# Performance work log

Measured on AMD Instinct MI355X. Metric: run time of the kernel, lower is better.

The kernel has to match this reference:

```python
import jax, jax.numpy as jnp
import numpy as np

B = 2048          # batch
F = 32            # input feature size
H = 512           # lstm hidden size
BN = 64           # autoencoder bottleneck
OUT = 8           # final dense output size
SEQ_LEN = 128
LOOK_AHEAD = 32
RS, RE = 0, 8     # replace_start, replace_end (RE-RS == OUT)


def setup_inputs() -> dict:
    key = jax.random.key(0)
    ks = jax.random.split(key, 16)
    s = lambda k, shape: (jax.random.normal(k, shape, jnp.float32) * 0.05)
    return {
        'x': jax.random.normal(ks[0], (B, SEQ_LEN + LOOK_AHEAD, F), jnp.float32),
        # layer-0 LSTMCell (input F)
        'Wih0': s(ks[1], (F, 4 * H)), 'Whh0': s(ks[2], (H, 4 * H)),
        'bih0': s(ks[3], (4 * H,)),   'bhh0': s(ks[4], (4 * H,)),
        # layer-1 LSTMCell (input H)
        'Wih1': s(ks[5], (H, 4 * H)), 'Whh1': s(ks[6], (H, 4 * H)),
        'bih1': s(ks[7], (4 * H,)),   'bhh1': s(ks[8], (4 * H,)),
        # discretizing autoencoder: 2H -> BN -> 2H (shared across layers)
        'We': s(ks[9], (2 * H, BN)),  'be': s(ks[10], (BN,)),
        'Wd': s(ks[11], (BN, 2 * H)), 'bd': s(ks[12], (2 * H,)),
        # final dense H -> OUT
        'Wf': s(ks[13], (H, OUT)),    'bf': s(ks[14], (OUT,)),
    }


def _lstm_cell(x, h, c, Wih, Whh, bih, bhh):
    # torch.nn.LSTMCell gate order: i, f, g, o
    g = x @ Wih + bih + h @ Whh + bhh          # [B, 4H]
    i, f, gg, o = jnp.split(g, 4, axis=1)
    i, f, o = jax.nn.sigmoid(i), jax.nn.sigmoid(f), jax.nn.sigmoid(o)
    c2 = f * c + i * jnp.tanh(gg)
    return o * jnp.tanh(c2), c2


def _ae(z, We, be, Wd, bd):
    # bottleneck with straight-through rounding (discretization)
    b = jnp.tanh(z @ We + be)
    q = b + jax.lax.stop_gradient(jnp.round(b) - b)
    return q @ Wd + bd


def _layers_fwd(x_t, st, p):
    h0, c0, h1, c1 = st
    hc = _ae(jnp.concatenate([h0, c0], axis=1), p['We'], p['be'], p['Wd'], p['bd'])
    h0, c0 = jnp.split(hc, 2, axis=1)
    h0, c0 = _lstm_cell(x_t, h0, c0, p['Wih0'], p['Whh0'], p['bih0'], p['bhh0'])
    # dropout layer between stacked layers is identity in eval mode
    hc = _ae(jnp.concatenate([h1, c1], axis=1), p['We'], p['be'], p['Wd'], p['bd'])
    h1, c1 = jnp.split(hc, 2, axis=1)
    h1, c1 = _lstm_cell(h0, h1, c1, p['Wih1'], p['Whh1'], p['bih1'], p['bhh1'])
    return (h0, c0, h1, c1)


def reference(x, Wih0, Whh0, bih0, bhh0, Wih1, Whh1, bih1, bhh1,
              We, be, Wd, bd, Wf, bf):
    p = dict(Wih0=Wih0, Whh0=Whh0, bih0=bih0, bhh0=bhh0,
             Wih1=Wih1, Whh1=Whh1, bih1=bih1, bhh1=bhh1,
             We=We, be=be, Wd=Wd, bd=bd)
    bsz = x.shape[0]
    z = jnp.zeros((bsz, H), x.dtype)
    st = (z, z, z, z)

    # warm-up phase over seq_len observed steps
    def step1(st, x_t):
        return _layers_fwd(x_t, st, p), None
    st, _ = jax.lax.scan(step1, st, jnp.swapaxes(x[:, :SEQ_LEN], 0, 1))
    out0 = st[2] @ Wf + bf  # final dense on top-layer h

    def step2(carry, x_t):
        st, out = carry
        x_t = x_t.at[:, RS:RE].set(out)
        st = _layers_fwd(x_t, st, p)
        out = st[2] @ Wf + bf
        return (st, out), out
    (_, _), outs = jax.lax.scan(step2, (st, out0),
                                jnp.swapaxes(x[:, SEQ_LEN:SEQ_LEN + LOOK_AHEAD], 0, 1))

    # [B, 1 + look_ahead, OUT]
    return jnp.concatenate([out0[:, None, :], jnp.swapaxes(outs, 0, 1)], axis=1)
```

## Files before the change

kernel.cpp:

```cpp
#include <hip/hip_runtime.h>
#include <math.h>

#define NB    2048
#define FIN   32
#define HH    512
#define G4    2048
#define BNE   64
#define OUTD  8
#define SEQL  128
#define LOOK  32
#define TOT   (SEQL + LOOK)
#define TB    8
#define NTHR  512

__device__ __forceinline__ float sigf(float v) { return 1.0f / (1.0f + expf(-v)); }

#define GMAC4(A, W)                                                     \
  { A[0].x = fmaf((W).x, hv.x, A[0].x); A[0].y = fmaf((W).y, hv.x, A[0].y); \
    A[1].x = fmaf((W).x, hv.y, A[1].x); A[1].y = fmaf((W).y, hv.y, A[1].y); \
    A[2].x = fmaf((W).x, hv.z, A[2].x); A[2].y = fmaf((W).y, hv.z, A[2].y); \
    A[3].x = fmaf((W).x, hv.w, A[3].x); A[3].y = fmaf((W).y, hv.w, A[3].y); }

__global__ __launch_bounds__(NTHR)
void fused_rnn(const float* __restrict__ x,
               const float* __restrict__ Wih0, const float* __restrict__ Whh0,
               const float* __restrict__ bih0, const float* __restrict__ bhh0,
               const float* __restrict__ Wih1, const float* __restrict__ Whh1,
               const float* __restrict__ bih1, const float* __restrict__ bhh1,
               const float* __restrict__ We,   const float* __restrict__ be,
               const float* __restrict__ Wd,   const float* __restrict__ bd,
               const float* __restrict__ Wf,   const float* __restrict__ bf,
               float* __restrict__ out)
{
  __shared__ float sh0[HH][TB], sc0[HH][TB], sh1[HH][TB], sc1[HH][TB];
  __shared__ float tq[2][BNE][TB];
  __shared__ float sx[FIN][TB];
  __shared__ float sout[TB][OUTD];

  const int t  = threadIdx.x;
  const int b0 = blockIdx.x * TB;

  for (int i = t; i < HH * TB; i += NTHR) {
    (&sh0[0][0])[i] = 0.f; (&sc0[0][0])[i] = 0.f;
    (&sh1[0][0])[i] = 0.f; (&sc1[0][0])[i] = 0.f;
  }

  const int q  = t & 255;
  const int sh = t >> 8;
  const int s4 = 4 * sh;
  const int u0 = 2 * q;
  float2 bg0[4], bg1[4];
#pragma unroll
  for (int m = 0; m < 4; m++) {
    const int c = m * HH + u0;
    bg0[m] = make_float2(bih0[c] + bhh0[c], bih0[c + 1] + bhh0[c + 1]);
    bg1[m] = make_float2(bih1[c] + bhh1[c], bih1[c + 1] + bhh1[c + 1]);
  }

  const int ae = t >> 8, n = t & 63, sp = (t >> 6) & 3;

  const float bdx = bd[2 * t], bdy = bd[2 * t + 1];

  const double Athr = 0.5493061443340549;

  for (int step = 0; step < TOT; ++step) {
    __syncthreads();

    {
      const float* Sh = ae ? &sh1[0][0] : &sh0[0][0];
      const float* Sc = ae ? &sc1[0][0] : &sc0[0][0];
      double a0 = (double)be[n], a1 = a0;
      const float* weh = We + n;
#pragma unroll 4
      for (int k = 0; k < HH; k++) {
        const float2 zz = *(const float2*)&Sh[k * TB + 2 * sp];
        const double wv = (double)weh[(size_t)k * BNE];
        a0 = fma((double)zz.x, wv, a0);
        a1 = fma((double)zz.y, wv, a1);
      }
      const float* wec = We + (size_t)HH * BNE + n;
#pragma unroll 4
      for (int k = 0; k < HH; k++) {
        const float2 zz = *(const float2*)&Sc[k * TB + 2 * sp];
        const double wv = (double)wec[(size_t)k * BNE];
        a0 = fma((double)zz.x, wv, a0);
        a1 = fma((double)zz.y, wv, a1);
      }
      tq[ae][n][2 * sp]     = (a0 > Athr) ? 1.f : ((a0 < -Athr) ? -1.f : 0.f);
      tq[ae][n][2 * sp + 1] = (a1 > Athr) ? 1.f : ((a1 < -Athr) ? -1.f : 0.f);
    }
    __syncthreads();

    {
      float2 d0[TB], d1[TB];
#pragma unroll
      for (int s = 0; s < TB; s++) { d0[s] = make_float2(bdx, bdy); d1[s] = d0[s]; }
      const float* wd = Wd + 2 * t;
#pragma unroll 2
      for (int j = 0; j < BNE; j++) {
        const float2 w = *(const float2*)&wd[(size_t)j * (2 * HH)];
        const float4 qA0 = *(const float4*)&tq[0][j][0];
        const float4 qB0 = *(const float4*)&tq[0][j][4];
        const float4 qA1 = *(const float4*)&tq[1][j][0];
        const float4 qB1 = *(const float4*)&tq[1][j][4];
        d0[0].x = fmaf(qA0.x, w.x, d0[0].x); d0[0].y = fmaf(qA0.x, w.y, d0[0].y);
        d0[1].x = fmaf(qA0.y, w.x, d0[1].x); d0[1].y = fmaf(qA0.y, w.y, d0[1].y);
        d0[2].x = fmaf(qA0.z, w.x, d0[2].x); d0[2].y = fmaf(qA0.z, w.y, d0[2].y);
        d0[3].x = fmaf(qA0.w, w.x, d0[3].x); d0[3].y = fmaf(qA0.w, w.y, d0[3].y);
        d0[4].x = fmaf(qB0.x, w.x, d0[4].x); d0[4].y = fmaf(qB0.x, w.y, d0[4].y);
        d0[5].x = fmaf(qB0.y, w.x, d0[5].x); d0[5].y = fmaf(qB0.y, w.y, d0[5].y);
        d0[6].x = fmaf(qB0.z, w.x, d0[6].x); d0[6].y = fmaf(qB0.z, w.y, d0[6].y);
        d0[7].x = fmaf(qB0.w, w.x, d0[7].x); d0[7].y = fmaf(qB0.w, w.y, d0[7].y);
        d1[0].x = fmaf(qA1.x, w.x, d1[0].x); d1[0].y = fmaf(qA1.x, w.y, d1[0].y);
        d1[1].x = fmaf(qA1.y, w.x, d1[1].x); d1[1].y = fmaf(qA1.y, w.y, d1[1].y);
        d1[2].x = fmaf(qA1.z, w.x, d1[2].x); d1[2].y = fmaf(qA1.z, w.y, d1[2].y);
        d1[3].x = fmaf(qA1.w, w.x, d1[3].x); d1[3].y = fmaf(qA1.w, w.y, d1[3].y);
        d1[4].x = fmaf(qB1.x, w.x, d1[4].x); d1[4].y = fmaf(qB1.x, w.y, d1[4].y);
        d1[5].x = fmaf(qB1.y, w.x, d1[5].x); d1[5].y = fmaf(qB1.y, w.y, d1[5].y);
        d1[6].x = fmaf(qB1.z, w.x, d1[6].x); d1[6].y = fmaf(qB1.z, w.y, d1[6].y);
        d1[7].x = fmaf(qB1.w, w.x, d1[7].x); d1[7].y = fmaf(qB1.w, w.y, d1[7].y);
      }
      if (t < 256) {
        const int u = 2 * t;
        *(float4*)&sh0[u][0]     = make_float4(d0[0].x, d0[1].x, d0[2].x, d0[3].x);
        *(float4*)&sh0[u][4]     = make_float4(d0[4].x, d0[5].x, d0[6].x, d0[7].x);
        *(float4*)&sh0[u + 1][0] = make_float4(d0[0].y, d0[1].y, d0[2].y, d0[3].y);
        *(float4*)&sh0[u + 1][4] = make_float4(d0[4].y, d0[5].y, d0[6].y, d0[7].y);
        *(float4*)&sh1[u][0]     = make_float4(d1[0].x, d1[1].x, d1[2].x, d1[3].x);
        *(float4*)&sh1[u][4]     = make_float4(d1[4].x, d1[5].x, d1[6].x, d1[7].x);
        *(float4*)&sh1[u + 1][0] = make_float4(d1[0].y, d1[1].y, d1[2].y, d1[3].y);
        *(float4*)&sh1[u + 1][4] = make_float4(d1[4].y, d1[5].y, d1[6].y, d1[7].y);
      } else {
        const int u = 2 * t - HH;
        *(float4*)&sc0[u][0]     = make_float4(d0[0].x, d0[1].x, d0[2].x, d0[3].x);
        *(float4*)&sc0[u][4]     = make_float4(d0[4].x, d0[5].x, d0[6].x, d0[7].x);
        *(float4*)&sc0[u + 1][0] = make_float4(d0[0].y, d0[1].y, d0[2].y, d0[3].y);
        *(float4*)&sc0[u + 1][4] = make_float4(d0[4].y, d0[5].y, d0[6].y, d0[7].y);
        *(float4*)&sc1[u][0]     = make_float4(d1[0].x, d1[1].x, d1[2].x, d1[3].x);
        *(float4*)&sc1[u][4]     = make_float4(d1[4].x, d1[5].x, d1[6].x, d1[7].x);
        *(float4*)&sc1[u + 1][0] = make_float4(d1[0].y, d1[1].y, d1[2].y, d1[3].y);
        *(float4*)&sc1[u + 1][4] = make_float4(d1[4].y, d1[5].y, d1[6].y, d1[7].y);
      }
      if (t < FIN * TB) {
        int s = t >> 5, f = t & 31;
        float xv;
        if (step >= SEQL && f < OUTD) xv = sout[s][f];
        else xv = x[((size_t)(b0 + s) * TOT + step) * FIN + f];
        sx[f][s] = xv;
      }
    }
    __syncthreads();

    {
      float2 gI[4], gF[4], gG[4], gO[4];
#pragma unroll
      for (int i = 0; i < 4; i++) { gI[i] = bg0[0]; gF[i] = bg0[1]; gG[i] = bg0[2]; gO[i] = bg0[3]; }
      {
        const float* row = Wih0 + u0;
#pragma unroll 4
        for (int k = 0; k < FIN; k++, row += G4) {
          const float2 wI = *(const float2*)(row);
          const float2 wF = *(const float2*)(row + HH);
          const float2 wG = *(const float2*)(row + 2 * HH);
          const float2 wO = *(const float2*)(row + 3 * HH);
          const float4 hv = *(const float4*)&sx[k][s4];
          GMAC4(gI, wI); GMAC4(gF, wF); GMAC4(gG, wG); GMAC4(gO, wO);
        }
      }
      {
        const float* row = Whh0 + u0;
#pragma unroll 8
        for (int k = 0; k < HH; k++, row += G4) {
          const float2 wI = *(const float2*)(row);
          const float2 wF = *(const float2*)(row + HH);
          const float2 wG = *(const float2*)(row + 2 * HH);
          const float2 wO = *(const float2*)(row + 3 * HH);
          const float4 hv = *(const float4*)&sh0[k][s4];
          GMAC4(gI, wI); GMAC4(gF, wF); GMAC4(gG, wG); GMAC4(gO, wO);
        }
      }
      const float4 cA = *(const float4*)&sc0[u0][s4];
      const float4 cB = *(const float4*)&sc0[u0 + 1][s4];
      const float coldA[4] = { cA.x, cA.y, cA.z, cA.w };
      const float coldB[4] = { cB.x, cB.y, cB.z, cB.w };
      float4 hnA, hnB, cnA, cnB;
      float* hA = (float*)&hnA; float* hB = (float*)&hnB;
      float* cnAp = (float*)&cnA; float* cnBp = (float*)&cnB;
#pragma unroll
      for (int i = 0; i < 4; i++) {
        float ig = sigf(gI[i].x), fg = sigf(gF[i].x);
        float gt = tanhf(gG[i].x), og = sigf(gO[i].x);
        float c2 = fmaf(fg, coldA[i], ig * gt);
        cnAp[i] = c2; hA[i] = og * tanhf(c2);
        ig = sigf(gI[i].y); fg = sigf(gF[i].y);
        gt = tanhf(gG[i].y); og = sigf(gO[i].y);
        c2 = fmaf(fg, coldB[i], ig * gt);
        cnBp[i] = c2; hB[i] = og * tanhf(c2);
      }
      __syncthreads();
      *(float4*)&sh0[u0][s4]     = hnA;
      *(float4*)&sh0[u0 + 1][s4] = hnB;
      *(float4*)&sc0[u0][s4]     = cnA;
      *(float4*)&sc0[u0 + 1][s4] = cnB;
    }
    __syncthreads();

    {
      float2 gI[4], gF[4], gG[4], gO[4];
#pragma unroll
      for (int i = 0; i < 4; i++) { gI[i] = bg1[0]; gF[i] = bg1[1]; gG[i] = bg1[2]; gO[i] = bg1[3]; }
      {
        const float* row = Wih1 + u0;
#pragma unroll 8
        for (int k = 0; k < HH; k++, row += G4) {
          const float2 wI = *(const float2*)(row);
          const float2 wF = *(const float2*)(row + HH);
          const float2 wG = *(const float2*)(row + 2 * HH);
          const float2 wO = *(const float2*)(row + 3 * HH);
          const float4 hv = *(const float4*)&sh0[k][s4];
          GMAC4(gI, wI); GMAC4(gF, wF); GMAC4(gG, wG); GMAC4(gO, wO);
        }
      }
      {
        const float* row = Whh1 + u0;
#pragma unroll 8
        for (int k = 0; k < HH; k++, row += G4) {
          const float2 wI = *(const float2*)(row);
          const float2 wF = *(const float2*)(row + HH);
          const float2 wG = *(const float2*)(row + 2 * HH);
          const float2 wO = *(const float2*)(row + 3 * HH);
          const float4 hv = *(const float4*)&sh1[k][s4];
          GMAC4(gI, wI); GMAC4(gF, wF); GMAC4(gG, wG); GMAC4(gO, wO);
        }
      }
      const float4 cA = *(const float4*)&sc1[u0][s4];
      const float4 cB = *(const float4*)&sc1[u0 + 1][s4];
      const float coldA[4] = { cA.x, cA.y, cA.z, cA.w };
      const float coldB[4] = { cB.x, cB.y, cB.z, cB.w };
      float4 hnA, hnB, cnA, cnB;
      float* hA = (float*)&hnA; float* hB = (float*)&hnB;
      float* cnAp = (float*)&cnA; float* cnBp = (float*)&cnB;
#pragma unroll
      for (int i = 0; i < 4; i++) {
        float ig = sigf(gI[i].x), fg = sigf(gF[i].x);
        float gt = tanhf(gG[i].x), og = sigf(gO[i].x);
        float c2 = fmaf(fg, coldA[i], ig * gt);
        cnAp[i] = c2; hA[i] = og * tanhf(c2);
        ig = sigf(gI[i].y); fg = sigf(gF[i].y);
        gt = tanhf(gG[i].y); og = sigf(gO[i].y);
        c2 = fmaf(fg, coldB[i], ig * gt);
        cnBp[i] = c2; hB[i] = og * tanhf(c2);
      }
      __syncthreads();
      *(float4*)&sh1[u0][s4]     = hnA;
      *(float4*)&sh1[u0 + 1][s4] = hnB;
      *(float4*)&sc1[u0][s4]     = cnA;
      *(float4*)&sc1[u0 + 1][s4] = cnB;
    }

    if (step >= SEQL - 1) {
      __syncthreads();
      if (t < TB * OUTD) {
        int s = t >> 3, o = t & 7;
        float a = bf[o];
#pragma unroll 4
        for (int k = 0; k < HH; k++) a = fmaf(sh1[k][s], Wf[k * OUTD + o], a);
        sout[s][o] = a;
        int slot = step - (SEQL - 1);
        out[((size_t)(b0 + s) * (1 + LOOK) + slot) * OUTD + o] = a;
      }
    }
  }
}

extern "C" void kernel_launch(void* const* d_in, const int* in_sizes, int n_in,
                              void* d_out, int out_size, void* d_ws, size_t ws_size,
                              hipStream_t stream) {
  const float* x    = (const float*)d_in[0];
  const float* Wih0 = (const float*)d_in[1];
  const float* Whh0 = (const float*)d_in[2];
  const float* bih0 = (const float*)d_in[3];
  const float* bhh0 = (const float*)d_in[4];
  const float* Wih1 = (const float*)d_in[5];
  const float* Whh1 = (const float*)d_in[6];
  const float* bih1 = (const float*)d_in[7];
  const float* bhh1 = (const float*)d_in[8];
  const float* We   = (const float*)d_in[9];
  const float* be   = (const float*)d_in[10];
  const float* Wd   = (const float*)d_in[11];
  const float* bd   = (const float*)d_in[12];
  const float* Wf   = (const float*)d_in[13];
  const float* bf   = (const float*)d_in[14];

  fused_rnn<<<NB / TB, NTHR, 0, stream>>>(x, Wih0, Whh0, bih0, bhh0,
                                          Wih1, Whh1, bih1, bhh1,
                                          We, be, Wd, bd, Wf, bf,
                                          (float*)d_out);
}
```

Baseline: 92.00 ms.

## Double batch tile per block to 16 rows with 1024 threads and remap AE work

Raises the per-block batch tile from 8 to 16 samples and the block size from 512 to 1024 threads. The encoder and decoder thread mappings are reworked: each encoder thread now handles one sample for both layers, and each decoder thread produces one output column for all 16 samples, one layer after the other. The aim is to reuse every weight load from global memory across more batch rows, halving total weight traffic, at the cost of fewer blocks (128), doubled shared memory per block, and possible register pressure. The unseen LSTM gate section must also be consistent with the new TB and NTHR.

```diff
diff --git a/kernel.cpp b/kernel.cpp
--- a/kernel.cpp
+++ b/kernel.cpp
@@ -10,8 +10,8 @@
 #define SEQL  128
 #define LOOK  32
 #define TOT   (SEQL + LOOK)
-#define TB    8
-#define NTHR  512
+#define TB    16
+#define NTHR  1024
 
 __device__ __forceinline__ float sigf(float v) { return 1.0f / (1.0f + expf(-v)); }
 
@@ -33,7 +33,7 @@
                float* __restrict__ out)
 {
   __shared__ float sh0[HH][TB], sc0[HH][TB], sh1[HH][TB], sc1[HH][TB];
-  __shared__ float tq[2][BNE][TB];
+  __shared__ float sq[2][BNE][TB];
   __shared__ float sx[FIN][TB];
   __shared__ float sout[TB][OUTD];
 
@@ -46,8 +46,8 @@
   }
 
   const int q  = t & 255;
-  const int sh = t >> 8;
-  const int s4 = 4 * sh;
+  const int v  = t >> 8;
+  const int s4 = 4 * v;
   const int u0 = 2 * q;
   float2 bg0[4], bg1[4];
 #pragma unroll
@@ -57,9 +57,9 @@
     bg1[m] = make_float2(bih1[c] + bhh1[c], bih1[c + 1] + bhh1[c + 1]);
   }
 
-  const int ae = t >> 8, n = t & 63, sp = (t >> 6) & 3;
-
-  const float bdx = bd[2 * t], bdy = bd[2 * t + 1];
+  const int n = t & 63, sE = t >> 6;
+
+  const float bdv = bd[t];
 
   const double Athr = 0.5493061443340549;
 
@@ -67,79 +67,76 @@
     __syncthreads();
 
     {
-      const float* Sh = ae ? &sh1[0][0] : &sh0[0][0];
-      const float* Sc = ae ? &sc1[0][0] : &sc0[0][0];
       double a0 = (double)be[n], a1 = a0;
       const float* weh = We + n;
 #pragma unroll 4
       for (int k = 0; k < HH; k++) {
-        const float2 zz = *(const float2*)&Sh[k * TB + 2 * sp];
         const double wv = (double)weh[(size_t)k * BNE];
-        a0 = fma((double)zz.x, wv, a0);
-        a1 = fma((double)zz.y, wv, a1);
+        a0 = fma((double)sh0[k][sE], wv, a0);
+        a1 = fma((double)sh1[k][sE], wv, a1);
       }
       const float* wec = We + (size_t)HH * BNE + n;
 #pragma unroll 4
       for (int k = 0; k < HH; k++) {
-        const float2 zz = *(const float2*)&Sc[k * TB + 2 * sp];
         const double wv = (double)wec[(size_t)k * BNE];
-        a0 = fma((double)zz.x, wv, a0);
-        a1 = fma((double)zz.y, wv, a1);
-      }
-      tq[ae][n][2 * sp]     = (a0 > Athr) ? 1.f : ((a0 < -Athr) ? -1.f : 0.f);
-      tq[ae][n][2 * sp + 1] = (a1 > Athr) ? 1.f : ((a1 < -Athr) ? -1.f : 0.f);
-    }
-    __syncthreads();
-
-    {
-      float2 d0[TB], d1[TB];
-#pragma unroll
-      for (int s = 0; s < TB; s++) { d0[s] = make_float2(bdx, bdy); d1[s] = d0[s]; }
-      const float* wd = Wd + 2 * t;
+        a0 = fma((double)sc0[k][sE], wv, a0);
+        a1 = fma((double)sc1[k][sE], wv, a1);
+      }
+      sq[0][n][sE] = (a0 > Athr) ? 1.f : ((a0 < -Athr) ? -1.f : 0.f);
+      sq[1][n][sE] = (a1 > Athr) ? 1.f : ((a1 < -Athr) ? -1.f : 0.f);
+    }
+    __syncthreads();
+
+    {
+      const float* wd = Wd + t;
+      float d[TB];
+#pragma unroll
+      for (int s = 0; s < TB; s++) d[s] = bdv;
 #pragma unroll 2
       for (int j = 0; j < BNE; j++) {
-        const float2 w = *(const float2*)&wd[(size_t)j * (2 * HH)];
-        const float4 qA0 = *(const float4*)&tq[0][j][0];
-        const float4 qB0 = *(const float4*)&tq[0][j][4];
-        const float4 qA1 = *(const float4*)&tq[1][j][0];
-        const float4 qB1 = *(const float4*)&tq[1][j][4];
-        d0[0].x = fmaf(qA0.x, w.x, d0[0].x); d0[0].y = fmaf(qA0.x, w.y, d0[0].y);
-        d0[1].x = fmaf(qA0.y, w.x, d0[1].x); d0[1].y = fmaf(qA0.y, w.y, d0[1].y);
-        d0[2].x = fmaf(qA0.z, w.x, d0[2].x); d0[2].y = fmaf(qA0.z, w.y, d0[2].y);
-        d0[3].x = fmaf(qA0.w, w.x, d0[3].x); d0[3].y = fmaf(qA0.w, w.y, d0[3].y);
-        d0[4].x = fmaf(qB0.x, w.x, d0[4].x); d0[4].y = fmaf(qB0.x, w.y, d0[4].y);
-        d0[5].x = fmaf(qB0.y, w.x, d0[5].x); d0[5].y = fmaf(qB0.y, w.y, d0[5].y);
-        d0[6].x = fmaf(qB0.z, w.x, d0[6].x); d0[6].y = fmaf(qB0.z, w.y, d0[6].y);
-        d0[7].x = fmaf(qB0.w, w.x, d0[7].x); d0[7].y = fmaf(qB0.w, w.y, d0[7].y);
-        d1[0].x = fmaf(qA1.x, w.x, d1[0].x); d1[0].y = fmaf(qA1.x, w.y, d1[0].y);
-        d1[1].x = fmaf(qA1.y, w.x, d1[1].x); d1[1].y = fmaf(qA1.y, w.y, d1[1].y);
-        d1[2].x = fmaf(qA1.z, w.x, d1[2].x); d1[2].y = fmaf(qA1.z, w.y, d1[2].y);
-        d1[3].x = fmaf(qA1.w, w.x, d1[3].x); d1[3].y = fmaf(qA1.w, w.y, d1[3].y);
-        d1[4].x = fmaf(qB1.x, w.x, d1[4].x); d1[4].y = fmaf(qB1.x, w.y, d1[4].y);
-        d1[5].x = fmaf(qB1.y, w.x, d1[5].x); d1[5].y = fmaf(qB1.y, w.y, d1[5].y);
-        d1[6].x = fmaf(qB1.z, w.x, d1[6].x); d1[6].y = fmaf(qB1.z, w.y, d1[6].y);
-        d1[7].x = fmaf(qB1.w, w.x, d1[7].x); d1[7].y = fmaf(qB1.w, w.y, d1[7].y);
-      }
-      if (t < 256) {
-        const int u = 2 * t;
-        *(float4*)&sh0[u][0]     = make_float4(d0[0].x, d0[1].x, d0[2].x, d0[3].x);
-        *(float4*)&sh0[u][4]     = make_float4(d0[4].x, d0[5].x, d0[6].x, d0[7].x);
-        *(float4*)&sh0[u + 1][0] = make_float4(d0[0].y, d0[1].y, d0[2].y, d0[3].y);
-        *(float4*)&sh0[u + 1][4] = make_float4(d0[4].y, d0[5].y, d0[6].y, d0[7].y);
-        *(float4*)&sh1[u][0]     = make_float4(d1[0].x, d1[1].x, d1[2].x, d1[3].x);
-        *(float4*)&sh1[u][4]     = make_float4(d1[4].x, d1[5].x, d1[6].x, d1[7].x);
-        *(float4*)&sh1[u + 1][0] = make_float4(d1[0].y, d1[1].y, d1[2].y, d1[3].y);
-        *(float4*)&sh1[u + 1][4] = make_float4(d1[4].y, d1[5].y, d1[6].y, d1[7].y);
-      } else {
-        const int u = 2 * t - HH;
-        *(float4*)&sc0[u][0]     = make_float4(d0[0].x, d0[1].x, d0[2].x, d0[3].x);
-        *(float4*)&sc0[u][4]     = make_float4(d0[4].x, d0[5].x, d0[6].x, d0[7].x);
-        *(float4*)&sc0[u + 1][0] = make_float4(d0[0].y, d0[1].y, d0[2].y, d0[3].y);
-        *(float4*)&sc0[u + 1][4] = make_float4(d0[4].y, d0[5].y, d0[6].y, d0[7].y);
-        *(float4*)&sc1[u][0]     = make_float4(d1[0].x, d1[1].x, d1[2].x, d1[3].x);
-        *(float4*)&sc1[u][4]     = make_float4(d1[4].x, d1[5].x, d1[6].x, d1[7].x);
-        *(float4*)&sc1[u + 1][0] = make_float4(d1[0].y, d1[1].y, d1[2].y, d1[3].y);
-        *(float4*)&sc1[u + 1][4] = make_float4(d1[4].y, d1[5].y, d1[6].y, d1[7].y);
+        const float w = wd[(size_t)j * (2 * HH)];
+        const float4 qA = *(const float4*)&sq[0][j][0];
+        const float4 qB = *(const float4*)&sq[0][j][4];
+        const float4 qC = *(const float4*)&sq[0][j][8];
+        const float4 qD = *(const float4*)&sq[0][j][12];
+        d[0]  = fmaf(qA.x, w, d[0]);  d[1]  = fmaf(qA.y, w, d[1]);
+        d[2]  = fmaf(qA.z, w, d[2]);  d[3]  = fmaf(qA.w, w, d[3]);
+        d[4]  = fmaf(qB.x, w, d[4]);  d[5]  = fmaf(qB.y, w, d[5]);
+        d[6]  = fmaf(qB.z, w, d[6]);  d[7]  = fmaf(qB.w, w, d[7]);
+        d[8]  = fmaf(qC.x, w, d[8]);  d[9]  = fmaf(qC.y, w, d[9]);
+        d[10] = fmaf(qC.z, w, d[10]); d[11] = fmaf(qC.w, w, d[11]);
+        d[12] = fmaf(qD.x, w, d[12]); d[13] = fmaf(qD.y, w, d[13]);
+        d[14] = fmaf(qD.z, w, d[14]); d[15] = fmaf(qD.w, w, d[15]);
+      }
+      {
+        float* dst = (t < HH) ? &sh0[t][0] : &sc0[t - HH][0];
+#pragma unroll
+        for (int s = 0; s < TB; s += 4)
+          *(float4*)&dst[s] = make_float4(d[s], d[s+1], d[s+2], d[s+3]);
+      }
+#pragma unroll
+      for (int s = 0; s < TB; s++) d[s] = bdv;
+#pragma unroll 2
+      for (int j = 0; j < BNE; j++) {
+        const float w = wd[(size_t)j * (2 * HH)];
+        const float4 qA = *(const float4*)&sq[1][j][0];
+        const float4 qB = *(const float4*)&sq[1][j][4];
+        const float4 qC = *(const float4*)&sq[1][j][8];
+        const float4 qD = *(const float4*)&sq[1][j][12];
+        d[0]  = fmaf(qA.x, w, d[0]);  d[1]  = fmaf(qA.y, w, d[1]);
+        d[2]  = fmaf(qA.z, w, d[2]);  d[3]  = fmaf(qA.w, w, d[3]);
+        d[4]  = fmaf(qB.x, w, d[4]);  d[5]  = fmaf(qB.y, w, d[5]);
+        d[6]  = fmaf(qB.z, w, d[6]);  d[7]  = fmaf(qB.w, w, d[7]);
+        d[8]  = fmaf(qC.x, w, d[8]);  d[9]  = fmaf(qC.y, w, d[9]);
+        d[10] = fmaf(qC.z, w, d[10]); d[11] = fmaf(qC.w, w, d[11]);
+        d[12] = fmaf(qD.x, w, d[12]); d[13] = fmaf(qD.y, w, d[13]);
+        d[14] = fmaf(qD.z, w, d[14]); d[15] = fmaf(qD.w, w, d[15]);
+      }
+      {
+        float* dst = (t < HH) ? &sh1[t][0] : &sc1[t - HH][0];
+#pragma unroll
+        for (int s = 0; s < TB; s += 4)
+          *(float4*)&dst[s] = make_float4(d[s], d[s+1], d[s+2], d[s+3]);
       }
       if (t < FIN * TB) {
         int s = t >> 5, f = t & 31;
```

Result: slower. 128.4 ms (+39.5%).
